# Optimization experiments

Hardware: AMD Instinct MI355X
Metric: run time of the kernel (lower is better)

## Reference

```python
import jax, jax.numpy as jnp
import numpy as np

B, S, F, D, H, L, K = 64, 512, 8, 512, 8, 2, 512
FF = 4 * D
DH = D // H


def _ln(x):
    m = jnp.mean(x, axis=-1, keepdims=True)
    v = jnp.var(x, axis=-1, keepdims=True)
    return (x - m) * jax.lax.rsqrt(v + 1e-5)


def _encoder_layer(x, Wqkv, Wo, W1, b1, W2, b2):
    # pre-LN multi-head self-attention
    h = _ln(x)
    qkv = h @ Wqkv                                   # [B,S,3D]
    q, k, v = jnp.split(qkv, 3, axis=-1)
    q = q.reshape(B, S, H, DH)
    k = k.reshape(B, S, H, DH)
    v = v.reshape(B, S, H, DH)
    scores = jnp.einsum('bqhd,bkhd->bhqk', q, k) / jnp.sqrt(jnp.float32(DH))
    attn = jax.nn.softmax(scores, axis=-1)
    o = jnp.einsum('bhqk,bkhd->bqhd', attn, v).reshape(B, S, D) @ Wo
    x = x + o
    # pre-LN feed-forward
    h = _ln(x)
    x = x + (jax.nn.relu(h @ W1 + b1) @ W2 + b2)
    return x


def setup_inputs() -> dict:
    key = jax.random.key(0)
    ks = jax.random.split(key, 12)
    sc = 0.02
    inp = {
        'x': jax.random.normal(ks[0], (B, S, F), dtype=jnp.float32),
        'enc_W': jax.random.normal(ks[1], (F, D), dtype=jnp.float32) * sc,
        'enc_b': jnp.zeros((D,), dtype=jnp.float32),
        'Wqkv': jax.random.normal(ks[2], (L, D, 3 * D), dtype=jnp.float32) * sc,
        'Wo': jax.random.normal(ks[3], (L, D, D), dtype=jnp.float32) * sc,
        'W1': jax.random.normal(ks[4], (L, D, FF), dtype=jnp.float32) * sc,
        'b1': jnp.zeros((L, FF), dtype=jnp.float32),
        'W2': jax.random.normal(ks[5], (L, FF, D), dtype=jnp.float32) * sc,
        'b2': jnp.zeros((L, D), dtype=jnp.float32),
        'centers': jax.random.normal(ks[6], (K, D), dtype=jnp.float32),
    }
    return inp


def reference(x, enc_W, enc_b, Wqkv, Wo, W1, b1, W2, b2, centers):
    # enc_embedding
    h = x @ enc_W + enc_b                            # [B,S,D]
    # seq_model: stack of standard transformer encoder layers
    for i in range(L):
        h = _encoder_layer(h, Wqkv[i], Wo[i], W1[i], b1[i], W2[i], b2[i])
    output_seq = h                                   # [B,S,D]
    # torch.cdist(output_seq, centers, p=2) via matmul expansion
    on2 = jnp.sum(output_seq * output_seq, axis=-1, keepdims=True)   # [B,S,1]
    cn2 = jnp.sum(centers * centers, axis=-1)                        # [K]
    dist2 = on2 + cn2[None, None, :] - 2.0 * jnp.einsum('bsd,kd->bsk', output_seq, centers)
    cluster_ids = jnp.argmin(dist2, axis=-1)                         # [B,S]
    assigned_centroids = centers[cluster_ids]                        # [B,S,D] gather
    diff = output_seq - assigned_centroids
    # torch.norm(diff, dim=1)**2 then mean == mean over (B,D) of sum over S of diff^2
    loss = jnp.mean(jnp.sum(diff * diff, axis=1))
    return loss, output_seq
```

## Files before the change

kernel.cpp:

```cpp
#include <hip/hip_runtime.h>
#include <cstdint>
#include <cstddef>

typedef __attribute__((ext_vector_type(4))) float f32x4;
typedef __attribute__((ext_vector_type(8))) short s16x8;
typedef __attribute__((ext_vector_type(4))) short s16x4;

__device__ __forceinline__ short f2bf(float f){
  unsigned u; __builtin_memcpy(&u, &f, 4);
  u += 0x7fffu + ((u >> 16) & 1u);
  return (short)(u >> 16);
}

__device__ __forceinline__ void gll16(const void* g, void* l) {
  auto* lp = (__attribute__((address_space(3))) unsigned*)(uintptr_t)(l);
  const auto* gp = (const __attribute__((address_space(1))) unsigned*)(uintptr_t)(g);
  __builtin_amdgcn_global_load_lds(gp, lp, 16, 0, 0);
}

__device__ __forceinline__ void ds_tr8(unsigned a, s16x4* r) {
  asm volatile(
    "ds_read_b64_tr_b16 %0, %8\n\t"
    "ds_read_b64_tr_b16 %1, %8 offset:512\n\t"
    "ds_read_b64_tr_b16 %2, %8 offset:2048\n\t"
    "ds_read_b64_tr_b16 %3, %8 offset:2560\n\t"
    "ds_read_b64_tr_b16 %4, %8 offset:4096\n\t"
    "ds_read_b64_tr_b16 %5, %8 offset:4608\n\t"
    "ds_read_b64_tr_b16 %6, %8 offset:6144\n\t"
    "ds_read_b64_tr_b16 %7, %8 offset:6656\n\t"
    "s_waitcnt lgkmcnt(0)"
    : "=&v"(r[0]), "=&v"(r[1]), "=&v"(r[2]), "=&v"(r[3]),
      "=&v"(r[4]), "=&v"(r[5]), "=&v"(r[6]), "=&v"(r[7])
    : "v"(a)
    : "memory");
}

__global__ __launch_bounds__(256) void encode_kernel(
    const float* __restrict__ x, const float* __restrict__ W,
    const float* __restrict__ b, float* __restrict__ out)
{
  const int t = blockIdx.x;
  float xv[8];
#pragma unroll
  for (int f = 0; f < 8; ++f) xv[f] = x[(size_t)t*8 + f];
  for (int d = threadIdx.x; d < 512; d += 256) {
    float acc = b[d];
#pragma unroll
    for (int f = 0; f < 8; ++f) acc += xv[f] * W[f*512 + d];
    out[(size_t)t*512 + d] = acc;
  }
}

__global__ __launch_bounds__(256) void ln_kernel(
    const float* __restrict__ x, short* __restrict__ out)
{
  const int w = threadIdx.x >> 6, lane = threadIdx.x & 63;
  const int t = blockIdx.x * 4 + w;
  const float* row = x + (size_t)t * 512;
  float4 v0 = *(const float4*)&row[lane*8];
  float4 v1 = *(const float4*)&row[lane*8 + 4];
  float vals[8] = {v0.x,v0.y,v0.z,v0.w,v1.x,v1.y,v1.z,v1.w};
  float s = 0.f, sq = 0.f;
#pragma unroll
  for (int i = 0; i < 8; ++i) { s += vals[i]; sq += vals[i]*vals[i]; }
#pragma unroll
  for (int m = 1; m < 64; m <<= 1) { s += __shfl_xor(s, m); sq += __shfl_xor(sq, m); }
  float mean = s * (1.f/512.f);
  float var  = sq * (1.f/512.f) - mean*mean;
  float rstd = rsqrtf(var + 1e-5f);
  s16x8 o;
#pragma unroll
  for (int i = 0; i < 8; ++i) o[i] = f2bf((vals[i]-mean)*rstd);
  *(s16x8*)&out[(size_t)t*512 + lane*8] = o;
}

__global__ __launch_bounds__(256) void transpose_bf16_kernel(
    const float* __restrict__ in, short* __restrict__ out, int K, int N, int kshift)
{
  const int o = blockIdx.x * 256 + threadIdx.x;
  const int k = o & (K - 1), n = o >> kshift;
  out[o] = f2bf(in[(size_t)k * N + n]);
}

__global__ __launch_bounds__(256) void convert_bf16_kernel(
    const float* __restrict__ in, short* __restrict__ out)
{
  const int i = blockIdx.x * 256 + threadIdx.x;
  out[i] = f2bf(in[i]);
}

__global__ __launch_bounds__(256) void packB_kernel(
    const float* __restrict__ in, short* __restrict__ out, int K, int N)
{
  const int n = blockIdx.x * 256 + threadIdx.x;
  const int k = blockIdx.y;
  const int ntk = K >> 5;
  const int idx = ((n >> 4) * ntk + (k >> 5)) * 512 + (((k >> 3) & 3) * 16 + (n & 15)) * 8 + (k & 7);
  out[idx] = f2bf(in[(size_t)k * N + n]);
}

template<bool BIAS, bool RELU, bool RESID, bool OUT32, bool FINAL>
__global__ __launch_bounds__(512, 1) void gemm_ldsb_kernel(
    const short* __restrict__ A, const short* __restrict__ Bt,
    void* Cout, const float* __restrict__ bias,
    const float* resid, short* __restrict__ obf, int M, int N, int K)
{
  __shared__ short As[4][256 * 32];
  __shared__ short Bs[4][256 * 32];
  const int tid = threadIdx.x;
  const int lane = tid & 63, w = tid >> 6;
  const int wr = w >> 2, wc = w & 3;
  const int q = lane & 15, g = lane >> 4;

  const int nx = gridDim.x;
  const int d = blockIdx.y * nx + blockIdx.x;
  const int per = (nx * gridDim.y) >> 3;
  const int lid = (d & 7) * per + (d >> 3);
  const int bx = lid % nx, by = lid / nx;
  const int m0 = by * 256, n0 = bx * 256;

  const int srow = lane >> 2;
  const int scol = (((lane & 3) ^ ((lane >> 4) & 3)) * 8);
  const short* aS0 = A  + (size_t)(m0 + w*32 + srow) * K + scol;
  const short* aS1 = aS0 + (size_t)16 * K;
  const short* bS0 = Bt + (size_t)(n0 + w*32 + srow) * K + scol;
  const short* bS1 = bS0 + (size_t)16 * K;
  const int d0 = (w*2) * 512, d1 = (w*2 + 1) * 512;
  const int gs = (g ^ (q >> 2)) * 8;

  f32x4 acc[8][4] = {};
  const int nt = K >> 5;

  auto STAGE = [&](int tt) {
    const int k0 = tt << 5, nb = tt & 3;
    gll16(aS0 + k0, &As[nb][d0]);
    gll16(aS1 + k0, &As[nb][d1]);
    gll16(bS0 + k0, &Bs[nb][d0]);
    gll16(bS1 + k0, &Bs[nb][d1]);
  };
  auto COMPUTE = [&](int t) {
    const int bufc = t & 3;
    if (t + 3 < nt) STAGE(t + 3);
    s16x8 aF[8], bF[4];
#pragma unroll
    for (int i = 0; i < 8; ++i) aF[i] = *(const s16x8*)&As[bufc][(wr*128 + i*16 + q)*32 + gs];
#pragma unroll
    for (int i = 0; i < 4; ++i) bF[i] = *(const s16x8*)&Bs[bufc][(wc*64 + i*16 + q)*32 + gs];
#pragma unroll
    for (int mi = 0; mi < 8; ++mi)
#pragma unroll
      for (int ni = 0; ni < 4; ++ni)
        acc[mi][ni] = __builtin_amdgcn_mfma_f32_16x16x32_bf16(aF[mi], bF[ni], acc[mi][ni], 0, 0, 0);
  };

  STAGE(0); STAGE(1); STAGE(2);

  for (int t = 0; t < nt - 2; ++t) {
    asm volatile("s_waitcnt vmcnt(8)" ::: "memory");
    __builtin_amdgcn_s_barrier();
    __builtin_amdgcn_sched_barrier(0);
    COMPUTE(t);
    __builtin_amdgcn_sched_barrier(0);
  }
  asm volatile("s_waitcnt vmcnt(4)" ::: "memory");
  __builtin_amdgcn_s_barrier();
  __builtin_amdgcn_sched_barrier(0);
  COMPUTE(nt - 2);
  asm volatile("s_waitcnt vmcnt(0)" ::: "memory");
  __builtin_amdgcn_s_barrier();
  __builtin_amdgcn_sched_barrier(0);
  COMPUTE(nt - 1);

#pragma unroll
  for (int mi = 0; mi < 8; ++mi) {
#pragma unroll
    for (int r = 0; r < 4; ++r) {
      const int gr = m0 + wr*128 + mi*16 + g*4 + r;
#pragma unroll
      for (int ni = 0; ni < 4; ++ni) {
        const int gc = n0 + wc*64 + ni*16 + q;
        float v = acc[mi][ni][r];
        if (BIAS) v += bias[gc];
        if (RELU) v = fmaxf(v, 0.f);
        if (RESID) v += resid[(size_t)gr * N + gc];
        const size_t idx = (size_t)gr * N + gc;
        if (FINAL) { ((float*)Cout)[idx] = v; obf[idx] = f2bf(v); }
        else if (OUT32) ((float*)Cout)[idx] = v;
        else ((short*)Cout)[idx] = f2bf(v);
      }
    }
  }
}

template<bool BIAS, bool RELU, bool RESID, bool OUT32>
__global__ __launch_bounds__(512, 1) void gemm_regb_kernel(
    const short* __restrict__ A, const short* __restrict__ Bp,
    void* Cout, const float* __restrict__ bias,
    const float* resid, int M, int N, int K)
{
  __shared__ short As[4][256 * 32];
  const int tid = threadIdx.x;
  const int lane = tid & 63, w = tid >> 6;
  const int wr = w >> 2, wc = w & 3;
  const int q = lane & 15, g = lane >> 4;

  const int nx = gridDim.x;
  const int d = blockIdx.y * nx + blockIdx.x;
  const int per = (nx * gridDim.y) >> 3;
  const int lid = (d & 7) * per + (d >> 3);
  const int bx = lid % nx, by = lid / nx;
  const int m0 = by * 256, n0 = bx * 256;

  const int srow = lane >> 2;
  const int scol = (((lane & 3) ^ ((lane >> 4) & 3)) * 8);
  const short* aS0 = A + (size_t)(m0 + w*32 + srow) * K + scol;
  const short* aS1 = aS0 + (size_t)16 * K;
  const int d0 = (w*2) * 512, d1 = (w*2 + 1) * 512;
  const int gs = (g ^ (q >> 2)) * 8;

  const int nt = K >> 5;
  const size_t bstep = (size_t)nt * 512;
  const short* bp0 = Bp + ((size_t)(n0 >> 4) + wc * 4) * bstep + lane * 8;

  f32x4 acc[8][4] = {};

  auto STAGE_A = [&](int tt) {
    const int k0 = tt << 5, nb = tt & 3;
    gll16(aS0 + k0, &As[nb][d0]);
    gll16(aS1 + k0, &As[nb][d1]);
  };
  s16x8 bA[4], bB[4];
  auto LOADB = [&](int tt, s16x8* bf) {
#pragma unroll
    for (int i = 0; i < 4; ++i)
      bf[i] = *(const s16x8*)&bp0[(size_t)i * bstep + (size_t)tt * 512];
  };
  auto TILE = [&](int t, s16x8* bcur, s16x8* bnxt, bool doLB, bool doSA) {
    __builtin_amdgcn_s_barrier();
    __builtin_amdgcn_sched_barrier(0);
    if (doLB) LOADB(t + 1, bnxt);
    __builtin_amdgcn_sched_barrier(0);
    if (doSA) STAGE_A(t + 3);
    __builtin_amdgcn_sched_barrier(0);
    const short* Ab = &As[t & 3][0];
    s16x8 aF[8];
#pragma unroll
    for (int i = 0; i < 8; ++i) aF[i] = *(const s16x8*)&Ab[(wr*128 + i*16 + q)*32 + gs];
    __builtin_amdgcn_s_setprio(1);
#pragma unroll
    for (int mi = 0; mi < 8; ++mi)
#pragma unroll
      for (int ni = 0; ni < 4; ++ni)
        acc[mi][ni] = __builtin_amdgcn_mfma_f32_16x16x32_bf16(aF[mi], bcur[ni], acc[mi][ni], 0, 0, 0);
    __builtin_amdgcn_s_setprio(0);
  };

  STAGE_A(0);
  LOADB(0, bA);
  STAGE_A(1);
  STAGE_A(2);

  for (int t = 0; t < nt - 2; t += 2) {
    asm volatile("s_waitcnt vmcnt(8)" ::: "memory");
    TILE(t, bA, bB, true, true);
    asm volatile("s_waitcnt vmcnt(8)" ::: "memory");
    TILE(t + 1, bB, bA, true, t + 4 < nt);
  }
  asm volatile("s_waitcnt vmcnt(6)" ::: "memory");
  TILE(nt - 2, bA, bB, true, false);
  asm volatile("s_waitcnt vmcnt(4)" ::: "memory");
  TILE(nt - 1, bB, bA, false, false);

#pragma unroll
  for (int mi = 0; mi < 8; ++mi) {
#pragma unroll
    for (int r = 0; r < 4; ++r) {
      const int gr = m0 + wr*128 + mi*16 + g*4 + r;
#pragma unroll
      for (int ni = 0; ni < 4; ++ni) {
        const int gc = n0 + wc*64 + ni*16 + q;
        float v = acc[mi][ni][r];
        if (BIAS) v += bias[gc];
        if (RELU) v = fmaxf(v, 0.f);
        if (RESID) v += resid[(size_t)gr * N + gc];
        if (OUT32) ((float*)Cout)[(size_t)gr * N + gc] = v;
        else       ((short*)Cout)[(size_t)gr * N + gc] = f2bf(v);
      }
    }
  }
}

__global__ __launch_bounds__(256) void attn_kernel(
    const short* __restrict__ qkv, short* __restrict__ attn_out)
{
  __shared__ short Ks[2][64 * 64];
  __shared__ short Vs[2][64 * 64];
  const int tid = threadIdx.x;
  const int w = tid >> 6, lane = tid & 63;
  const int q16 = lane & 15, g = lane >> 4;
  const int dd = blockIdx.x;
  const int lid = (dd & 7) * (int)(gridDim.x >> 3) + (dd >> 3);
  const int qt4 = lid & 7, h = (lid >> 3) & 7, b = lid >> 6;
  const size_t base = (size_t)b * 512 * 1536;
  const int qrow = qt4*64 + w*16 + q16;

  s16x8 bQ0, bQ1;
  {
    const size_t p = base + (size_t)qrow * 1536 + h*64 + g*8;
    bQ0 = *(const s16x8*)&qkv[p];
    bQ1 = *(const s16x8*)&qkv[p + 32];
  }

  const int c0 = w*2, c1 = w*2 + 1;
  const short* kS0 = qkv + base + (size_t)(c0*8 + (lane>>3))*1536 + 512 + h*64 + ((lane&7)^(lane>>3))*8;
  const short* kS1 = qkv + base + (size_t)(c1*8 + (lane>>3))*1536 + 512 + h*64 + ((lane&7)^(lane>>3))*8;
  const short* vS0 = qkv + base + (size_t)((c0&1)*32 + (lane>>1))*1536 + 1024 + h*64 + (c0>>1)*16 + (lane&1)*8;
  const short* vS1 = qkv + base + (size_t)((c1&1)*32 + (lane>>1))*1536 + 1024 + h*64 + (c1>>1)*16 + (lane&1)*8;

  const unsigned vs_lane = (unsigned)(size_t)(&Vs[0][0]) + (unsigned)((q16 + g*64)*2);
  const int sw = q16 & 7;

  float mrun = -1e30f, ssum = 0.f;
  f32x4 O[4] = {};

  gll16(kS0, &Ks[0][c0*512]);
  gll16(kS1, &Ks[0][c1*512]);
  gll16(vS0, &Vs[0][c0*512]);
  gll16(vS1, &Vs[0][c1*512]);
  __syncthreads();

  int cur = 0;
  for (int j0 = 0; j0 < 512; j0 += 64) {
    s16x8 ka0[4], ka1[4];
#pragma unroll
    for (int grp = 0; grp < 4; ++grp) {
      const int rb = (grp*16 + q16) * 64;
      ka0[grp] = *(const s16x8*)&Ks[cur][rb + ((g    ) ^ sw)*8];
      ka1[grp] = *(const s16x8*)&Ks[cur][rb + ((g + 4) ^ sw)*8];
    }
    if (j0 + 64 < 512) {
      const size_t joff = (size_t)(j0 + 64) * 1536;
      const int nxt = cur ^ 1;
      gll16(kS0 + joff, &Ks[nxt][c0*512]);
      gll16(kS1 + joff, &Ks[nxt][c1*512]);
      gll16(vS0 + joff, &Vs[nxt][c0*512]);
      gll16(vS1 + joff, &Vs[nxt][c1*512]);
    }
    __builtin_amdgcn_sched_barrier(0);

    f32x4 c[4];
    __builtin_amdgcn_s_setprio(1);
#pragma unroll
    for (int grp = 0; grp < 4; ++grp) {
      f32x4 z = {};
      c[grp] = __builtin_amdgcn_mfma_f32_16x16x32_bf16(ka0[grp], bQ0, z, 0, 0, 0);
      c[grp] = __builtin_amdgcn_mfma_f32_16x16x32_bf16(ka1[grp], bQ1, c[grp], 0, 0, 0);
    }
    __builtin_amdgcn_s_setprio(0);

    float sc[16];
#pragma unroll
    for (int grp = 0; grp < 4; ++grp)
#pragma unroll
      for (int r = 0; r < 4; ++r) sc[grp*4 + r] = c[grp][r] * 0.125f;
    float bm = sc[0];
#pragma unroll
    for (int i = 1; i < 16; ++i) bm = fmaxf(bm, sc[i]);
    bm = fmaxf(bm, __shfl_xor(bm, 16));
    bm = fmaxf(bm, __shfl_xor(bm, 32));
    const float mn = fmaxf(mrun, bm);
    const float alpha = __expf(mrun - mn);
    float p[16]; float bs = 0.f;
#pragma unroll
    for (int i = 0; i < 16; ++i) { p[i] = __expf(sc[i] - mn); bs += p[i]; }
    bs += __shfl_xor(bs, 16);
    bs += __shfl_xor(bs, 32);
    ssum = ssum * alpha + bs;
    mrun = mn;
#pragma unroll
    for (int db = 0; db < 4; ++db) O[db] *= alpha;

#pragma unroll
    for (int kk = 0; kk < 2; ++kk) {
      s16x8 pf;
#pragma unroll
      for (int e = 0; e < 8; ++e) pf[e] = f2bf(p[(kk*2 + (e >> 2))*4 + (e & 3)]);
      s16x4 r[8];
      ds_tr8(vs_lane + (unsigned)(cur << 13) + (unsigned)(kk*1024), r);
      __builtin_amdgcn_sched_barrier(0);
      __builtin_amdgcn_s_setprio(1);
#pragma unroll
      for (int db = 0; db < 4; ++db) {
        s16x8 vf = __builtin_shufflevector(r[2*db], r[2*db + 1], 0, 1, 2, 3, 4, 5, 6, 7);
        O[db] = __builtin_amdgcn_mfma_f32_16x16x32_bf16(vf, pf, O[db], 0, 0, 0);
      }
      __builtin_amdgcn_s_setprio(0);
    }
    __syncthreads();
    cur ^= 1;
  }

  const float inv = 1.f / ssum;
  const size_t tok = (size_t)b*512 + qrow;
#pragma unroll
  for (int db = 0; db < 4; ++db) {
    s16x4 ov;
#pragma unroll
    for (int r = 0; r < 4; ++r) ov[r] = f2bf(O[db][r] * inv);
    *(s16x4*)&attn_out[tok*512 + h*64 + db*16 + g*4] = ov;
  }
}

__global__ __launch_bounds__(256) void cn2_kernel(
    const float* __restrict__ centers, float* __restrict__ cn2)
{
  const int c = blockIdx.x;
  __shared__ float red[256];
  float s = 0.f;
  for (int d = threadIdx.x; d < 512; d += 256) { float v = centers[(size_t)c*512 + d]; s += v*v; }
  red[threadIdx.x] = s; __syncthreads();
  for (int off = 128; off > 0; off >>= 1) {
    if (threadIdx.x < off) red[threadIdx.x] += red[threadIdx.x + off];
    __syncthreads();
  }
  if (threadIdx.x == 0) cn2[c] = red[0];
}

__global__ __launch_bounds__(256) void argmin_kernel(
    const float* __restrict__ gdist, const float* __restrict__ cn2,
    const float* __restrict__ seq, const float* __restrict__ centers,
    float* __restrict__ partial)
{
  const int w = threadIdx.x >> 6, lane = threadIdx.x & 63;
  const int t = blockIdx.x * 4 + w;
  float best = 1e30f; int bi = 0;
#pragma unroll
  for (int j = 0; j < 8; ++j) {
    const int k = j*64 + lane;
    const float v = cn2[k] - 2.f * gdist[(size_t)t*512 + k];
    if (v < best || (v == best && k < bi)) { best = v; bi = k; }
  }
#pragma unroll
  for (int mm = 1; mm < 64; mm <<= 1) {
    const float ov = __shfl_xor(best, mm); const int oi = __shfl_xor(bi, mm);
    if (ov < best || (ov == best && oi < bi)) { best = ov; bi = oi; }
  }
  float s = 0.f;
#pragma unroll
  for (int j = 0; j < 8; ++j) {
    const int dcol = j*64 + lane;
    const float o = seq[(size_t)t*512 + dcol];
    const float c = centers[(size_t)bi*512 + dcol];
    const float dv = o - c;
    s += dv * dv;
  }
#pragma unroll
  for (int mm = 1; mm < 64; mm <<= 1) s += __shfl_xor(s, mm);
  __shared__ float red[4];
  if (lane == 0) red[w] = s;
  __syncthreads();
  if (threadIdx.x == 0) partial[blockIdx.x] = red[0] + red[1] + red[2] + red[3];
}

__global__ __launch_bounds__(256) void loss_kernel(
    const float* __restrict__ partial, int n, float* __restrict__ out)
{
  float s = 0.f;
  for (int i = threadIdx.x; i < n; i += 256) s += partial[i];
  __shared__ float red[256];
  red[threadIdx.x] = s; __syncthreads();
  for (int off = 128; off > 0; off >>= 1) {
    if (threadIdx.x < off) red[threadIdx.x] += red[threadIdx.x + off];
    __syncthreads();
  }
  if (threadIdx.x == 0) out[0] = red[0] * (1.f / 32768.f);
}

extern "C" void kernel_launch(void* const* d_in, const int* in_sizes, int n_in,
                              void* d_out, int out_size, void* d_ws, size_t ws_size,
                              hipStream_t stream) {
  const float* x     = (const float*)d_in[0];
  const float* enc_W = (const float*)d_in[1];
  const float* enc_b = (const float*)d_in[2];
  const float* Wqkv  = (const float*)d_in[3];
  const float* Wo    = (const float*)d_in[4];
  const float* W1    = (const float*)d_in[5];
  const float* b1    = (const float*)d_in[6];
  const float* W2    = (const float*)d_in[7];
  const float* b2    = (const float*)d_in[8];
  const float* cen   = (const float*)d_in[9];
  float* out = (float*)d_out;

  const int NT = 32768;
  char* ws = (char*)d_ws;
  float* resid   = (float*)(ws);
  short* h_ln    = (short*)(ws + 67108864);
  char*  pool    = ws + 100663296;
  short* qkv     = (short*)pool;
  short* attn_o  = (short*)(pool + 100663296);
  short* hidden  = (short*)pool;
  float* gdist   = (float*)pool;
  short* wbase   = (short*)(ws + 234881024);
  short* wqP     = wbase;
  short* woT     = wbase + 1572864;
  short* w1P     = wbase + 2097152;
  short* w2T     = wbase + 4194304;
  short* cenb    = wbase + 6291456;
  float* cn2     = (float*)(ws + 247988224);
  float* partial = (float*)(ws + 247990272);

  for (int l = 0; l < 2; ++l) {
    packB_kernel<<<dim3(6, 512), 256, 0, stream>>>(Wqkv + (size_t)l*512*1536, wqP + (size_t)l*786432, 512, 1536);
    transpose_bf16_kernel<<<1024, 256, 0, stream>>>(Wo  + (size_t)l*512*512,  woT + (size_t)l*262144, 512, 512, 9);
    packB_kernel<<<dim3(8, 512), 256, 0, stream>>>(W1   + (size_t)l*512*2048, w1P + (size_t)l*1048576, 512, 2048);
    transpose_bf16_kernel<<<4096, 256, 0, stream>>>(W2  + (size_t)l*2048*512, w2T + (size_t)l*1048576, 2048, 512, 11);
  }
  convert_bf16_kernel<<<1024, 256, 0, stream>>>(cen, cenb);
  cn2_kernel<<<512, 256, 0, stream>>>(cen, cn2);

  encode_kernel<<<NT, 256, 0, stream>>>(x, enc_W, enc_b, resid);

  for (int l = 0; l < 2; ++l) {
    ln_kernel<<<NT/4, 256, 0, stream>>>(resid, h_ln);
    gemm_regb_kernel<false,false,false,false><<<dim3(6, 128), 512, 0, stream>>>(
        h_ln, wqP + (size_t)l*786432, qkv, nullptr, nullptr, NT, 1536, 512);
    attn_kernel<<<4096, 256, 0, stream>>>(qkv, attn_o);
    gemm_ldsb_kernel<false,false,true,true,false><<<dim3(2, 128), 512, 0, stream>>>(
        attn_o, woT + (size_t)l*262144, resid, nullptr, resid, nullptr, NT, 512, 512);
    ln_kernel<<<NT/4, 256, 0, stream>>>(resid, h_ln);
    gemm_regb_kernel<true,true,false,false><<<dim3(8, 128), 512, 0, stream>>>(
        h_ln, w1P + (size_t)l*1048576, hidden, b1 + (size_t)l*2048, nullptr, NT, 2048, 512);
    if (l == 0) {
      gemm_ldsb_kernel<true,false,true,true,false><<<dim3(2, 128), 512, 0, stream>>>(
          hidden, w2T + (size_t)l*1048576, resid, b2 + (size_t)l*512, resid, nullptr, NT, 512, 2048);
    } else {
      gemm_ldsb_kernel<true,false,true,true,true><<<dim3(2, 128), 512, 0, stream>>>(
          hidden, w2T + (size_t)l*1048576, out + 1, b2 + (size_t)l*512, resid, h_ln, NT, 512, 2048);
    }
  }

  gemm_ldsb_kernel<false,false,false,true,false><<<dim3(2, 128), 512, 0, stream>>>(
      h_ln, cenb, gdist, nullptr, nullptr, nullptr, NT, 512, 512);
  argmin_kernel<<<NT/4, 256, 0, stream>>>(gdist, cn2, out + 1, cen, partial);
  loss_kernel<<<1, 256, 0, stream>>>(partial, NT/4, out);
}
```

Baseline: 920.6 us.

## Rewrite LDS-staged GEMM as 8-phase pipelined K=64 double-buffered kernel

Replaces the 4-stage K=32 LDS GEMM with a double-buffered K=64 tile schedule. Each iteration is split into four compute phases of MFMA work, and global-to-LDS loads for the next tiles are interleaved between them. Barriers, s_setprio and an XOR swizzle on the new 64-wide row layout are meant to overlap memory traffic with MFMA and avoid LDS bank conflicts. The schedule adds more barriers per iteration, and the hand-placed vmcnt waits and prefetch logic are delicate to get right.

New measurement: 905.7 us. No clear change (-1.6%).

```diff
diff --git a/kernel.cpp b/kernel.cpp
--- a/kernel.cpp
+++ b/kernel.cpp
@@ -100,17 +100,17 @@
 }
 
 template<bool BIAS, bool RELU, bool RESID, bool OUT32, bool FINAL>
-__global__ __launch_bounds__(512, 1) void gemm_ldsb_kernel(
+__global__ __launch_bounds__(512, 1) void gemm_8ph_kernel(
     const short* __restrict__ A, const short* __restrict__ Bt,
     void* Cout, const float* __restrict__ bias,
     const float* resid, short* __restrict__ obf, int M, int N, int K)
 {
-  __shared__ short As[4][256 * 32];
-  __shared__ short Bs[4][256 * 32];
+  __shared__ short As[2][2][8192];
+  __shared__ short Bs[2][2][8192];
   const int tid = threadIdx.x;
   const int lane = tid & 63, w = tid >> 6;
   const int wr = w >> 2, wc = w & 3;
-  const int q = lane & 15, g = lane >> 4;
+  const int q = lane & 15, gl = lane >> 4;
 
   const int nx = gridDim.x;
   const int d = blockIdx.y * nx + blockIdx.x;
@@ -119,63 +119,100 @@
   const int bx = lid % nx, by = lid / nx;
   const int m0 = by * 256, n0 = bx * 256;
 
-  const int srow = lane >> 2;
-  const int scol = (((lane & 3) ^ ((lane >> 4) & 3)) * 8);
-  const short* aS0 = A  + (size_t)(m0 + w*32 + srow) * K + scol;
-  const short* aS1 = aS0 + (size_t)16 * K;
-  const short* bS0 = Bt + (size_t)(n0 + w*32 + srow) * K + scol;
-  const short* bS1 = bS0 + (size_t)16 * K;
-  const int d0 = (w*2) * 512, d1 = (w*2 + 1) * 512;
-  const int gs = (g ^ (q >> 2)) * 8;
+  const int r_lo = tid >> 3, sp = tid & 7;
+  const int scol = (sp ^ (r_lo & 7)) * 8;
+  const int ldst = tid * 8;
+
+  auto STA = [&](int kt, int h) {
+    short* dst = &As[kt & 1][h][ldst];
+    const short* s = A + (size_t)(m0 + h*128 + r_lo) * K + (kt << 6) + scol;
+    gll16(s, dst);
+    gll16(s + (size_t)64 * K, dst + 4096);
+  };
+  auto STB = [&](int kt, int h) {
+    short* dst = &Bs[kt & 1][h][ldst];
+    const short* s = Bt + (size_t)(n0 + h*128 + r_lo) * K + (kt << 6) + scol;
+    gll16(s, dst);
+    gll16(s + (size_t)64 * K, dst + 4096);
+  };
+
+  const int x0 = ( gl      ^ (q & 7)) * 8;
+  const int x1 = ((gl + 4) ^ (q & 7)) * 8;
+  const int aoff = q * 64;
+  const int boff = ((wc & 1) * 64 + q) * 64;
+  const int bh = wc >> 1;
 
   f32x4 acc[8][4] = {};
-  const int nt = K >> 5;
-
-  auto STAGE = [&](int tt) {
-    const int k0 = tt << 5, nb = tt & 3;
-    gll16(aS0 + k0, &As[nb][d0]);
-    gll16(aS1 + k0, &As[nb][d1]);
-    gll16(bS0 + k0, &Bs[nb][d0]);
-    gll16(bS1 + k0, &Bs[nb][d1]);
-  };
-  auto COMPUTE = [&](int t) {
-    const int bufc = t & 3;
-    if (t + 3 < nt) STAGE(t + 3);
-    s16x8 aF[8], bF[4];
-#pragma unroll
-    for (int i = 0; i < 8; ++i) aF[i] = *(const s16x8*)&As[bufc][(wr*128 + i*16 + q)*32 + gs];
-#pragma unroll
-    for (int i = 0; i < 4; ++i) bF[i] = *(const s16x8*)&Bs[bufc][(wc*64 + i*16 + q)*32 + gs];
-#pragma unroll
-    for (int mi = 0; mi < 8; ++mi)
-#pragma unroll
-      for (int ni = 0; ni < 4; ++ni)
-        acc[mi][ni] = __builtin_amdgcn_mfma_f32_16x16x32_bf16(aF[mi], bF[ni], acc[mi][ni], 0, 0, 0);
-  };
-
-  STAGE(0); STAGE(1); STAGE(2);
-
-  for (int t = 0; t < nt - 2; ++t) {
-    asm volatile("s_waitcnt vmcnt(8)" ::: "memory");
+  const int NT = K >> 6;
+
+#define ARD(dst, mi, ks) dst = *(const s16x8*)&Awr[(mi)*1024 + aoff + ((ks) ? x1 : x0)]
+#define BRD(dst, ni, ks) dst = *(const s16x8*)&Bh_[(ni)*1024 + boff + ((ks) ? x1 : x0)]
+#define MM(mi, ni, af0, af1) \
+  acc[mi][ni] = __builtin_amdgcn_mfma_f32_16x16x32_bf16(af0, bF[(ni)*2],   acc[mi][ni], 0, 0, 0); \
+  acc[mi][ni] = __builtin_amdgcn_mfma_f32_16x16x32_bf16(af1, bF[(ni)*2+1], acc[mi][ni], 0, 0, 0)
+#define BARS { __builtin_amdgcn_s_barrier(); __builtin_amdgcn_sched_barrier(0); }
+
+  STA(0,0); STA(0,1); STB(0,0); STB(0,1);
+  STA(1,0); STA(1,1); STB(1,0); STB(1,1);
+  asm volatile("s_waitcnt vmcnt(8)" ::: "memory");
+  __builtin_amdgcn_sched_barrier(0);
+  __builtin_amdgcn_s_barrier();
+
+  for (int u = 0; u < NT; ++u) {
+    const short* Awr = &As[u & 1][wr][0];
+    const short* Bh_ = &Bs[u & 1][bh][0];
+    s16x8 aF[8], bF[8];
+    if (u >= 1 && u + 1 < NT) STA(u + 1, 0);
+    ARD(aF[0],0,0); ARD(aF[1],0,1); ARD(aF[2],1,0); ARD(aF[3],1,1);
+    ARD(aF[4],2,0); ARD(aF[5],2,1); ARD(aF[6],3,0); ARD(aF[7],3,1);
+    BRD(bF[0],0,0); BRD(bF[1],0,1); BRD(bF[2],1,0); BRD(bF[3],1,1);
+    BARS;
+    __builtin_amdgcn_s_setprio(1);
+    MM(0,0,aF[0],aF[1]); MM(1,0,aF[2],aF[3]); MM(2,0,aF[4],aF[5]); MM(3,0,aF[6],aF[7]);
+    MM(0,1,aF[0],aF[1]); MM(1,1,aF[2],aF[3]); MM(2,1,aF[4],aF[5]); MM(3,1,aF[6],aF[7]);
+    __builtin_amdgcn_s_setprio(0);
+    BARS;
+    if (u >= 1 && u + 1 < NT) STA(u + 1, 1);
+    BRD(bF[4],2,0); BRD(bF[5],2,1); BRD(bF[6],3,0); BRD(bF[7],3,1);
+    BARS;
+    __builtin_amdgcn_s_setprio(1);
+    MM(0,2,aF[0],aF[1]); MM(1,2,aF[2],aF[3]); MM(2,2,aF[4],aF[5]); MM(3,2,aF[6],aF[7]);
+    MM(0,3,aF[0],aF[1]); MM(1,3,aF[2],aF[3]); MM(2,3,aF[4],aF[5]); MM(3,3,aF[6],aF[7]);
+    __builtin_amdgcn_s_setprio(0);
+    BARS;
+    if (u + 2 < NT) STB(u + 2, 0);
+    ARD(aF[0],4,0); ARD(aF[1],4,1); ARD(aF[2],5,0); ARD(aF[3],5,1);
+    ARD(aF[4],6,0); ARD(aF[5],6,1); ARD(aF[6],7,0); ARD(aF[7],7,1);
+    BARS;
+    __builtin_amdgcn_s_setprio(1);
+    MM(4,0,aF[0],aF[1]); MM(5,0,aF[2],aF[3]); MM(6,0,aF[4],aF[5]); MM(7,0,aF[6],aF[7]);
+    MM(4,1,aF[0],aF[1]); MM(5,1,aF[2],aF[3]); MM(6,1,aF[4],aF[5]); MM(7,1,aF[6],aF[7]);
+    __builtin_amdgcn_s_setprio(0);
+    BARS;
+    if (u + 2 < NT) STB(u + 2, 1);
+    BARS;
+    __builtin_amdgcn_s_setprio(1);
+    MM(4,2,aF[0],aF[1]); MM(5,2,aF[2],aF[3]); MM(6,2,aF[4],aF[5]); MM(7,2,aF[6],aF[7]);
+    MM(4,3,aF[0],aF[1]); MM(5,3,aF[2],aF[3]); MM(6,3,aF[4],aF[5]); MM(7,3,aF[6],aF[7]);
+    __builtin_amdgcn_s_setprio(0);
+    if (u + 1 < NT) {
+      if (u + 2 < NT) asm volatile("s_waitcnt vmcnt(4)" ::: "memory");
+      else            asm volatile("s_waitcnt vmcnt(0)" ::: "memory");
+    }
+    __builtin_amdgcn_sched_barrier(0);
     __builtin_amdgcn_s_barrier();
     __builtin_amdgcn_sched_barrier(0);
-    COMPUTE(t);
-    __builtin_amdgcn_sched_barrier(0);
-  }
-  asm volatile("s_waitcnt vmcnt(4)" ::: "memory");
-  __builtin_amdgcn_s_barrier();
-  __builtin_amdgcn_sched_barrier(0);
-  COMPUTE(nt - 2);
-  asm volatile("s_waitcnt vmcnt(0)" ::: "memory");
-  __builtin_amdgcn_s_barrier();
-  __builtin_amdgcn_sched_barrier(0);
-  COMPUTE(nt - 1);
+  }
+#undef ARD
+#undef BRD
+#undef MM
+#undef BARS
 
 #pragma unroll
   for (int mi = 0; mi < 8; ++mi) {
 #pragma unroll
     for (int r = 0; r < 4; ++r) {
-      const int gr = m0 + wr*128 + mi*16 + g*4 + r;
+      const int gr = m0 + wr*128 + mi*16 + gl*4 + r;
 #pragma unroll
       for (int ni = 0; ni < 4; ++ni) {
         const int gc = n0 + wc*64 + ni*16 + q;
@@ -525,21 +562,21 @@
     gemm_regb_kernel<false,false,false,false><<<dim3(6, 128), 512, 0, stream>>>(
         h_ln, wqP + (size_t)l*786432, qkv, nullptr, nullptr, NT, 1536, 512);
     attn_kernel<<<4096, 256, 0, stream>>>(qkv, attn_o);
-    gemm_ldsb_kernel<false,false,true,true,false><<<dim3(2, 128), 512, 0, stream>>>(
+    gemm_8ph_kernel<false,false,true,true,false><<<dim3(2, 128), 512, 0, stream>>>(
         attn_o, woT + (size_t)l*262144, resid, nullptr, resid, nullptr, NT, 512, 512);
     ln_kernel<<<NT/4, 256, 0, stream>>>(resid, h_ln);
     gemm_regb_kernel<true,true,false,false><<<dim3(8, 128), 512, 0, stream>>>(
         h_ln, w1P + (size_t)l*1048576, hidden, b1 + (size_t)l*2048, nullptr, NT, 2048, 512);
     if (l == 0) {
-      gemm_ldsb_kernel<true,false,true,true,false><<<dim3(2, 128), 512, 0, stream>>>(
+      gemm_8ph_kernel<true,false,true,true,false><<<dim3(2, 128), 512, 0, stream>>>(
           hidden, w2T + (size_t)l*1048576, resid, b2 + (size_t)l*512, resid, nullptr, NT, 512, 2048);
     } else {
-      gemm_ldsb_kernel<true,false,true,true,true><<<dim3(2, 128), 512, 0, stream>>>(
+      gemm_8ph_kernel<true,false,true,true,true><<<dim3(2, 128), 512, 0, stream>>>(
           hidden, w2T + (size_t)l*1048576, out + 1, b2 + (size_t)l*512, resid, h_ln, NT, 512, 2048);
     }
   }
 
-  gemm_ldsb_kernel<false,false,false,true,false><<<dim3(2, 128), 512, 0, stream>>>(
+  gemm_8ph_kernel<false,false,false,true,false><<<dim3(2, 128), 512, 0, stream>>>(
       h_ln, cenb, gdist, nullptr, nullptr, nullptr, NT, 512, 512);
   argmin_kernel<<<NT/4, 256, 0, stream>>>(gdist, cn2, out + 1, cen, partial);
   loss_kernel<<<1, 256, 0, stream>>>(partial, NT/4, out);
```
